# Kernel tuning notes

Hardware: AMD Instinct MI355X
Metric: run time of the kernel (lower is better)

## Reference

```python
import jax, jax.numpy as jnp
import numpy as np

B, S, D = 4, 4096, 64

def setup_inputs() -> dict:
    key = jax.random.key(0)
    kq, kk, kv, km = jax.random.split(key, 4)
    q = jax.random.normal(kq, (B, S, D), dtype=jnp.float32)
    k = jax.random.normal(kk, (B, S, D), dtype=jnp.float32)
    v = jax.random.normal(kv, (B, S, D), dtype=jnp.float32)
    # binary keep-mask in {0,1}; log(mask) -> {0, -inf}
    mask = (jax.random.uniform(km, (B, S)) > 0.2).astype(jnp.float32)
    return {"q": q, "k": k, "v": v, "mask": mask}

def reference(q, k, v, mask):
    emb_dim = q.shape[-1]
    qs = q / jnp.asarray(emb_dim, q.dtype) ** 0.5           # [B,S,D] scaled query
    scores = jnp.einsum('bqd,bkd->bqk', qs, k)              # [B,S,S]
    scores = scores + jnp.log(mask)[:, None, :]             # mask keys via log-add
    w = jax.nn.softmax(scores, axis=-1)                     # [B,S,S]
    out = jnp.einsum('bqk,bkd->bqd', w, v)                  # [B,S,D]
    # post-blend: masked query positions pass through the (scaled) query
    return out * mask[..., None] + qs * (1.0 - mask)[..., None]
```

## Files before the change

kernel.cpp:

```cpp
#include <hip/hip_runtime.h>
#include <hip/hip_bf16.h>

#define BATCH 4
#define SEQ   4096
#define DIM   64
#define TK    64
#define TOTQ  (BATCH * SEQ)
#define LOG2E 1.4426950408889634f

#if __has_builtin(__builtin_amdgcn_mfma_f32_16x16x16bf16_1k)
#define HAVE_1K 1
#else
#define HAVE_1K 0
#endif

#if __has_builtin(__builtin_amdgcn_exp2f)
#define EXP2(x) __builtin_amdgcn_exp2f(x)
#else
#define EXP2(x) exp2f(x)
#endif

typedef __attribute__((ext_vector_type(8))) short bf16x8;
typedef __attribute__((ext_vector_type(4))) short bf16x4;
typedef __attribute__((ext_vector_type(4))) float f32x4;

#define AS1 __attribute__((address_space(1)))
#define AS3 __attribute__((address_space(3)))

static __device__ __forceinline__ short f2bf(float x) {
    __hip_bfloat16 h = __float2bfloat16(x);
    return *reinterpret_cast<short*>(&h);
}
static __device__ __forceinline__ float bf2f(short s) {
    unsigned int u = ((unsigned int)(unsigned short)s) << 16;
    float f; __builtin_memcpy(&f, &u, 4); return f;
}
static __device__ __forceinline__ int pk2bf(float lo, float hi) {
    __hip_bfloat162 t = __float22bfloat162_rn(make_float2(lo, hi));
    int r; __builtin_memcpy(&r, &t, 4); return r;
}
static __device__ __forceinline__ bf16x4 mk4(const f32x4& s) {
    int2 t = make_int2(pk2bf(s[0], s[1]), pk2bf(s[2], s[3]));
    bf16x4 r; __builtin_memcpy(&r, &t, 8); return r;
}
static __device__ __forceinline__ f32x4 mfma16(bf16x4 a, bf16x4 b, f32x4 c) {
#if HAVE_1K
    return __builtin_amdgcn_mfma_f32_16x16x16bf16_1k(a, b, c, 0, 0, 0);
#else
    asm("v_mfma_f32_16x16x16_bf16 %0, %1, %2, %0" : "+v"(c) : "v"(a), "v"(b));
    return c;
#endif
}
static __device__ __forceinline__ void async16(const short* g, short* l) {
    __builtin_amdgcn_global_load_lds((const AS1 unsigned int*)g,
                                     (AS3 unsigned int*)l, 16, 0, 0);
}

__global__ __launch_bounds__(256)
void pack_kv(const float* __restrict__ kg, const float* __restrict__ vg,
             const float* __restrict__ mg,
             short* __restrict__ kp, short* __restrict__ vtp)
{
    if (blockIdx.x < 256) {
        #pragma unroll
        for (int i = 0; i < 4; ++i) {
            const int unit = blockIdx.x * 1024 + i * 256 + threadIdx.x;
            const int row = unit >> 4;
            const int d0  = (unit & 15) * 4;
            f32x4 kv = *reinterpret_cast<const f32x4*>(kg + (size_t)row * DIM + d0);
            short4 ks;
            ks.x = f2bf(kv[0]); ks.y = f2bf(kv[1]); ks.z = f2bf(kv[2]); ks.w = f2bf(kv[3]);
            const int gs = (d0 >> 3) ^ (row & 7);
            *reinterpret_cast<short4*>(kp + (size_t)row * DIM + gs * 8 + (d0 & 7)) = ks;
        }
    } else {
        __shared__ float Vl[64][66];
        __shared__ float Ml[64];
        const int tile = blockIdx.x - 256;
        const float* src = vg + (size_t)tile * TK * DIM;
        const int tid = threadIdx.x;
        #pragma unroll
        for (int i = 0; i < 4; ++i) {
            int idx = i * 256 + tid;
            int key = idx >> 4, part = idx & 15;
            f32x4 vv = *reinterpret_cast<const f32x4*>(src + (size_t)key * DIM + part * 4);
            float2* p0 = reinterpret_cast<float2*>(&Vl[key][part * 4]);
            p0[0] = make_float2(vv[0], vv[1]);
            p0[1] = make_float2(vv[2], vv[3]);
        }
        if (tid < 64) Ml[tid] = mg[(size_t)tile * TK + tid];
        __syncthreads();
        #pragma unroll
        for (int i = 0; i < 2; ++i) {
            const int gid = i * 256 + tid;
            const int d = gid >> 3;
            const int G = gid & 7;
            const int qd = G >> 1, u = G & 1;
            alignas(16) short s8[8];
            #pragma unroll
            for (int e = 0; e < 8; ++e) {
                const int v = e >> 2, j = e & 3;
                const int key = (2 * u + v) * 16 + qd * 4 + j;
                s8[e] = f2bf(Vl[key][d] * Ml[key]);
            }
            const int Gs = G ^ (d & 7);
            short* dst = vtp + (size_t)tile * (TK * DIM) + d * TK + Gs * 8;
            *reinterpret_cast<int4*>(dst) = *reinterpret_cast<const int4*>(s8);
        }
    }
}

template<int NSEG>
__global__ __launch_bounds__(256, 4)
void attn_fwd8(const float* __restrict__ qg, const float* __restrict__ mg,
               const short* __restrict__ kp, const short* __restrict__ vtp,
               float* __restrict__ outg,
               short* __restrict__ Opart, float* __restrict__ lpart)
{
    constexpr int SEGLEN = SEQ / NSEG;
    constexpr int ITERS  = SEGLEN / TK;

    __shared__ __align__(16) short Kl[2][TK][DIM];
    __shared__ __align__(16) short Vt[2][DIM][TK];

    const int tid  = threadIdx.x;
    const int wave = tid >> 6;
    const int lane = tid & 63;
    const int ln   = lane & 15;
    const int quad = lane >> 4;

    const int qblk = blockIdx.x & 31;
    const int rest = blockIdx.x >> 5;
    const int seg  = (NSEG == 1) ? 0 : (rest & (NSEG - 1));
    const int b    = (NSEG == 1) ? rest : (rest / NSEG);

    const int qw = qblk * 128 + wave * 32;
    const size_t bbase = (size_t)b * SEQ * DIM;

    const short* kb  = kp  + bbase + (size_t)seg * SEGLEN * DIM;
    const short* vb  = vtp + bbase + (size_t)seg * SEGLEN * DIM;
    const float* mgb = mg + (size_t)b * SEQ;

    const int gs0 = quad ^ (ln & 7);

    bf16x8 aq[2][2];
    #pragma unroll
    for (int qt = 0; qt < 2; ++qt) {
        const float* qrow = qg + bbase + (size_t)(qw + qt * 16 + ln) * DIM;
        #pragma unroll
        for (int h = 0; h < 2; ++h) {
            alignas(16) short tmp[8];
            #pragma unroll
            for (int j = 0; j < 8; ++j)
                tmp[j] = f2bf(qrow[quad * 8 + h * 32 + j] * (0.125f * LOG2E));
            aq[qt][h] = *reinterpret_cast<bf16x8*>(tmp);
        }
    }

    f32x4 O[2][4];
    float lacc[2] = {0.f, 0.f};
    #pragma unroll
    for (int qt = 0; qt < 2; ++qt)
        #pragma unroll
        for (int i = 0; i < 4; ++i) O[qt][i] = (f32x4){0.f, 0.f, 0.f, 0.f};

    #pragma unroll
    for (int i = 0; i < 2; ++i) {
        const int c = wave * 2 + i;
        async16(kb + c * 512 + lane * 8, &Kl[0][0][0] + c * 512);
        async16(vb + c * 512 + lane * 8, &Vt[0][0][0] + c * 512);
    }

    for (int t = 0; t < ITERS; ++t) {
        const int buf = t & 1;
        asm volatile("s_waitcnt vmcnt(0)" ::: "memory");
        __syncthreads();

        if (t + 1 < ITERS) {
            const short* gk = kb + (size_t)(t + 1) * TK * DIM;
            const short* gv = vb + (size_t)(t + 1) * TK * DIM;
            #pragma unroll
            for (int i = 0; i < 2; ++i) {
                const int c = wave * 2 + i;
                async16(gk + c * 512 + lane * 8, &Kl[buf ^ 1][0][0] + c * 512);
                async16(gv + c * 512 + lane * 8, &Vt[buf ^ 1][0][0] + c * 512);
            }
        }

        const int key0 = seg * SEGLEN + t * TK;
        const short* klb = &Kl[buf][0][0];
        const short* vtb = &Vt[buf][0][0];

        #pragma unroll
        for (int u = 0; u < 2; ++u) {
            f32x4 m4[2];
            #pragma unroll
            for (int v = 0; v < 2; ++v)
                m4[v] = *reinterpret_cast<const f32x4*>(
                    mgb + key0 + (2 * u + v) * 16 + quad * 4);

            f32x4 sf[2][2];
            #pragma unroll
            for (int v = 0; v < 2; ++v) {
                const int s = 2 * u + v;
                bf16x8 ka0 = *reinterpret_cast<const bf16x8*>(
                    klb + (s * 16 + ln) * DIM + gs0 * 8);
                bf16x8 ka1 = *reinterpret_cast<const bf16x8*>(
                    klb + (s * 16 + ln) * DIM + (gs0 ^ 4) * 8);
                #pragma unroll
                for (int qt = 0; qt < 2; ++qt) {
                    f32x4 acc = (f32x4){0.f, 0.f, 0.f, 0.f};
                    acc = __builtin_amdgcn_mfma_f32_16x16x32_bf16(ka0, aq[qt][0], acc, 0, 0, 0);
                    acc = __builtin_amdgcn_mfma_f32_16x16x32_bf16(ka1, aq[qt][1], acc, 0, 0, 0);
                    sf[qt][v] = acc;
                }
            }

            bf16x4 bp[2][2];
            #pragma unroll
            for (int qt = 0; qt < 2; ++qt) {
                #pragma unroll
                for (int v = 0; v < 2; ++v) {
                    #pragma unroll
                    for (int r = 0; r < 4; ++r) {
                        sf[qt][v][r] = EXP2(sf[qt][v][r]);
                        lacc[qt] = fmaf(sf[qt][v][r], m4[v][r], lacc[qt]);
                    }
                    bp[qt][v] = mk4(sf[qt][v]);
                }
            }

            const int gvu = (quad * 2 + u) ^ (ln & 7);
            #pragma unroll
            for (int ds = 0; ds < 4; ++ds) {
                bf16x8 vf = *reinterpret_cast<const bf16x8*>(
                    vtb + (ds * 16 + ln) * TK + gvu * 8);
                bf16x4 va0 = __builtin_shufflevector(vf, vf, 0, 1, 2, 3);
                bf16x4 va1 = __builtin_shufflevector(vf, vf, 4, 5, 6, 7);
                #pragma unroll
                for (int qt = 0; qt < 2; ++qt) {
                    O[qt][ds] = mfma16(va0, bp[qt][0], O[qt][ds]);
                    O[qt][ds] = mfma16(va1, bp[qt][1], O[qt][ds]);
                }
            }
        }
    }

    #pragma unroll
    for (int qt = 0; qt < 2; ++qt) {
        lacc[qt] += __shfl_xor(lacc[qt], 16);
        lacc[qt] += __shfl_xor(lacc[qt], 32);
    }

    if (NSEG == 1) {
        #pragma unroll
        for (int qt = 0; qt < 2; ++qt) {
            const int qrow_i = qw + qt * 16 + ln;
            const float qm = mgb[qrow_i];
            const float inv = 1.0f / lacc[qt];
            const float* qrow = qg + bbase + (size_t)qrow_i * DIM;
            float* orow = outg + bbase + (size_t)qrow_i * DIM;
            #pragma unroll
            for (int ds = 0; ds < 4; ++ds) {
                const int d0 = ds * 16 + quad * 4;
                f32x4 o4;
                #pragma unroll
                for (int r = 0; r < 4; ++r) o4[r] = O[qt][ds][r] * inv;
                if (qm == 0.0f) {
                    f32x4 q4 = *reinterpret_cast<const f32x4*>(qrow + d0);
                    #pragma unroll
                    for (int r = 0; r < 4; ++r) o4[r] = q4[r] * 0.125f;
                }
                *reinterpret_cast<f32x4*>(orow + d0) = o4;
            }
        }
    } else {
        #pragma unroll
        for (int qt = 0; qt < 2; ++qt) {
            const int gq = b * SEQ + qw + qt * 16 + ln;
            short* ob = Opart + ((size_t)seg * TOTQ + gq) * 64;
            #pragma unroll
            for (int ds = 0; ds < 2; ++ds) {
                bf16x4 lo = mk4(O[qt][ds * 2 + 0]);
                bf16x4 hi = mk4(O[qt][ds * 2 + 1]);
                *reinterpret_cast<bf16x4*>(ob + (ds * 2 + 0) * 16 + quad * 4) = lo;
                *reinterpret_cast<bf16x4*>(ob + (ds * 2 + 1) * 16 + quad * 4) = hi;
            }
            if (quad == 0) lpart[(size_t)seg * TOTQ + gq] = lacc[qt];
        }
    }
}

template<int NSEG>
__global__ __launch_bounds__(256)
void combine_p(const short* __restrict__ Opart, const float* __restrict__ lpart,
               const float* __restrict__ qg, const float* __restrict__ mg,
               float* __restrict__ outg)
{
    const int t = blockIdx.x * 256 + threadIdx.x;
    const int gq = t >> 4;
    const int d0 = (t & 15) * 4;
    float a0 = 0.f, a1 = 0.f, a2 = 0.f, a3 = 0.f, den = 0.f;
    #pragma unroll
    for (int s = 0; s < NSEG; ++s) {
        const short* ob = Opart + ((size_t)s * TOTQ + gq) * 64 + d0;
        short4 o4 = *reinterpret_cast<const short4*>(ob);
        a0 += bf2f(o4.x); a1 += bf2f(o4.y);
        a2 += bf2f(o4.z); a3 += bf2f(o4.w);
        den += lpart[(size_t)s * TOTQ + gq];
    }
    const float inv = 1.0f / den;
    f32x4 o;
    o[0] = a0 * inv; o[1] = a1 * inv; o[2] = a2 * inv; o[3] = a3 * inv;
    if (mg[gq] == 0.0f) {
        f32x4 q4 = *reinterpret_cast<const f32x4*>(qg + (size_t)gq * DIM + d0);
        #pragma unroll
        for (int r = 0; r < 4; ++r) o[r] = q4[r] * 0.125f;
    }
    *reinterpret_cast<f32x4*>(outg + (size_t)gq * DIM + d0) = o;
}

extern "C" void kernel_launch(void* const* d_in, const int* in_sizes, int n_in,
                              void* d_out, int out_size, void* d_ws, size_t ws_size,
                              hipStream_t stream) {
    (void)in_sizes; (void)n_in; (void)out_size;
    const float* q = (const float*)d_in[0];
    const float* k = (const float*)d_in[1];
    const float* v = (const float*)d_in[2];
    const float* m = (const float*)d_in[3];
    float* out = (float*)d_out;

    const size_t nelem  = (size_t)BATCH * SEQ * DIM;
    const size_t packsz = nelem * 2 * sizeof(short);
    const size_t osz    = (size_t)8 * TOTQ * 64 * sizeof(short);
    const size_t lsz    = (size_t)8 * TOTQ * sizeof(float);

    short* kp  = (short*)d_ws;
    short* vtp = kp + nelem;
    short* Op  = (short*)((char*)d_ws + packsz);
    float* lp  = (float*)((char*)d_ws + packsz + osz);

    pack_kv<<<dim3(512), dim3(256), 0, stream>>>(k, v, m, kp, vtp);

    if (ws_size >= packsz + osz + lsz) {
        attn_fwd8<8><<<dim3(BATCH * 32 * 8), dim3(256), 0, stream>>>(
            q, m, kp, vtp, out, Op, lp);
        combine_p<8><<<dim3(TOTQ * 16 / 256), dim3(256), 0, stream>>>(
            Op, lp, q, m, out);
    } else {
        attn_fwd8<1><<<dim3(BATCH * 32), dim3(256), 0, stream>>>(
            q, m, kp, vtp, out, nullptr, nullptr);
    }
}
```

Baseline: 104.9 us.

## Halve key tile to 32, double split-K segments to 16, raise occupancy

Shrinks the per-iteration key tile from 64 to 32 keys, which also changes the packed transposed-V layout and its swizzle. The number of key segments grows from 8 to 16, doubling the grid, and launch bounds now ask for 8 blocks per CU to improve occupancy and latency hiding. The trade-off is twice as many partial outputs written and read by the combine kernel, more loop iterations and barriers per key, and a larger workspace requirement.

```diff
diff --git a/kernel.cpp b/kernel.cpp
--- a/kernel.cpp
+++ b/kernel.cpp
@@ -4,8 +4,9 @@
 #define BATCH 4
 #define SEQ   4096
 #define DIM   64
-#define TK    64
+#define TK    32
 #define TOTQ  (BATCH * SEQ)
+#define NSEG  16
 #define LOG2E 1.4426950408889634f
 
 #if __has_builtin(__builtin_amdgcn_mfma_f32_16x16x16bf16_1k)
@@ -76,8 +77,8 @@
     } else {
         __shared__ float Vl[64][66];
         __shared__ float Ml[64];
-        const int tile = blockIdx.x - 256;
-        const float* src = vg + (size_t)tile * TK * DIM;
+        const int t64 = blockIdx.x - 256;
+        const float* src = vg + (size_t)t64 * 64 * DIM;
         const int tid = threadIdx.x;
         #pragma unroll
         for (int i = 0; i < 4; ++i) {
@@ -88,36 +89,36 @@
             p0[0] = make_float2(vv[0], vv[1]);
             p0[1] = make_float2(vv[2], vv[3]);
         }
-        if (tid < 64) Ml[tid] = mg[(size_t)tile * TK + tid];
+        if (tid < 64) Ml[tid] = mg[(size_t)t64 * 64 + tid];
         __syncthreads();
         #pragma unroll
         for (int i = 0; i < 2; ++i) {
             const int gid = i * 256 + tid;
-            const int d = gid >> 3;
-            const int G = gid & 7;
-            const int qd = G >> 1, u = G & 1;
+            const int t2 = gid >> 8;
+            const int d  = (gid >> 2) & 63;
+            const int G  = gid & 3;
             alignas(16) short s8[8];
             #pragma unroll
             for (int e = 0; e < 8; ++e) {
                 const int v = e >> 2, j = e & 3;
-                const int key = (2 * u + v) * 16 + qd * 4 + j;
+                const int key = t2 * 32 + v * 16 + G * 4 + j;
                 s8[e] = f2bf(Vl[key][d] * Ml[key]);
             }
-            const int Gs = G ^ (d & 7);
-            short* dst = vtp + (size_t)tile * (TK * DIM) + d * TK + Gs * 8;
+            const int Gs = G ^ ((d >> 1) & 3);
+            short* dst = vtp + ((size_t)t64 * 2 + t2) * (TK * DIM) + d * TK + Gs * 8;
             *reinterpret_cast<int4*>(dst) = *reinterpret_cast<const int4*>(s8);
         }
     }
 }
 
-template<int NSEG>
-__global__ __launch_bounds__(256, 4)
-void attn_fwd8(const float* __restrict__ qg, const float* __restrict__ mg,
+template<int NS>
+__global__ __launch_bounds__(256, 8)
+void attn_fwd9(const float* __restrict__ qg, const float* __restrict__ mg,
                const short* __restrict__ kp, const short* __restrict__ vtp,
                float* __restrict__ outg,
                short* __restrict__ Opart, float* __restrict__ lpart)
 {
-    constexpr int SEGLEN = SEQ / NSEG;
+    constexpr int SEGLEN = SEQ / NS;
     constexpr int ITERS  = SEGLEN / TK;
 
     __shared__ __align__(16) short Kl[2][TK][DIM];
@@ -131,8 +132,8 @@
 
     const int qblk = blockIdx.x & 31;
     const int rest = blockIdx.x >> 5;
-    const int seg  = (NSEG == 1) ? 0 : (rest & (NSEG - 1));
-    const int b    = (NSEG == 1) ? rest : (rest / NSEG);
+    const int seg  = (NS == 1) ? 0 : (rest & (NS - 1));
+    const int b    = (NS == 1) ? rest : (rest / NS);
 
     const int qw = qblk * 128 + wave * 32;
     const size_t bbase = (size_t)b * SEQ * DIM;
@@ -142,6 +143,7 @@
     const float* mgb = mg + (size_t)b * SEQ;
 
     const int gs0 = quad ^ (ln & 7);
+    const int gsv = quad ^ ((ln >> 1) & 3);
 
     bf16x8 aq[2][2];
     #pragma unroll
@@ -164,12 +166,8 @@
         #pragma unroll
         for (int i = 0; i < 4; ++i) O[qt][i] = (f32x4){0.f, 0.f, 0.f, 0.f};
 
-    #pragma unroll
-    for (int i = 0; i < 2; ++i) {
-        const int c = wave * 2 + i;
-        async16(kb + c * 512 + lane * 8, &Kl[0][0][0] + c * 512);
-        async16(vb + c * 512 + lane * 8, &Vt[0][0][0] + c * 512);
-    }
+    async16(kb + wave * 512 + lane * 8, &Kl[0][0][0] + wave * 512);
+    async16(vb + wave * 512 + lane * 8, &Vt[0][0][0] + wave * 512);
 
     for (int t = 0; t < ITERS; ++t) {
         const int buf = t & 1;
@@ -179,69 +177,59 @@
         if (t + 1 < ITERS) {
             const short* gk = kb + (size_t)(t + 1) * TK * DIM;
             const short* gv = vb + (size_t)(t + 1) * TK * DIM;
-            #pragma unroll
-            for (int i = 0; i < 2; ++i) {
-                const int c = wave * 2 + i;
-                async16(gk + c * 512 + lane * 8, &Kl[buf ^ 1][0][0] + c * 512);
-                async16(gv + c * 512 + lane * 8, &Vt[buf ^ 1][0][0] + c * 512);
-            }
+            async16(gk + wave * 512 + lane * 8, &Kl[buf ^ 1][0][0] + wave * 512);
+            async16(gv + wave * 512 + lane * 8, &Vt[buf ^ 1][0][0] + wave * 512);
         }
 
         const int key0 = seg * SEGLEN + t * TK;
         const short* klb = &Kl[buf][0][0];
         const short* vtb = &Vt[buf][0][0];
 
-        #pragma unroll
-        for (int u = 0; u < 2; ++u) {
-            f32x4 m4[2];
-            #pragma unroll
-            for (int v = 0; v < 2; ++v)
-                m4[v] = *reinterpret_cast<const f32x4*>(
-                    mgb + key0 + (2 * u + v) * 16 + quad * 4);
-
-            f32x4 sf[2][2];
+        f32x4 m4[2];
+        #pragma unroll
+        for (int v = 0; v < 2; ++v)
+            m4[v] = *reinterpret_cast<const f32x4*>(mgb + key0 + v * 16 + quad * 4);
+
+        f32x4 sf[2][2];
+        #pragma unroll
+        for (int v = 0; v < 2; ++v) {
+            bf16x8 ka0 = *reinterpret_cast<const bf16x8*>(
+                klb + (v * 16 + ln) * DIM + gs0 * 8);
+            bf16x8 ka1 = *reinterpret_cast<const bf16x8*>(
+                klb + (v * 16 + ln) * DIM + (gs0 ^ 4) * 8);
+            #pragma unroll
+            for (int qt = 0; qt < 2; ++qt) {
+                f32x4 acc = (f32x4){0.f, 0.f, 0.f, 0.f};
+                acc = __builtin_amdgcn_mfma_f32_16x16x32_bf16(ka0, aq[qt][0], acc, 0, 0, 0);
+                acc = __builtin_amdgcn_mfma_f32_16x16x32_bf16(ka1, aq[qt][1], acc, 0, 0, 0);
+                sf[qt][v] = acc;
+            }
+        }
+
+        bf16x4 bp[2][2];
+        #pragma unroll
+        for (int qt = 0; qt < 2; ++qt) {
             #pragma unroll
             for (int v = 0; v < 2; ++v) {
-                const int s = 2 * u + v;
-                bf16x8 ka0 = *reinterpret_cast<const bf16x8*>(
-                    klb + (s * 16 + ln) * DIM + gs0 * 8);
-                bf16x8 ka1 = *reinterpret_cast<const bf16x8*>(
-                    klb + (s * 16 + ln) * DIM + (gs0 ^ 4) * 8);
                 #pragma unroll
-                for (int qt = 0; qt < 2; ++qt) {
-                    f32x4 acc = (f32x4){0.f, 0.f, 0.f, 0.f};
-                    acc = __builtin_amdgcn_mfma_f32_16x16x32_bf16(ka0, aq[qt][0], acc, 0, 0, 0);
-                    acc = __builtin_amdgcn_mfma_f32_16x16x32_bf16(ka1, aq[qt][1], acc, 0, 0, 0);
-                    sf[qt][v] = acc;
+                for (int r = 0; r < 4; ++r) {
+                    sf[qt][v][r] = EXP2(sf[qt][v][r]);
+                    lacc[qt] = fmaf(sf[qt][v][r], m4[v][r], lacc[qt]);
                 }
-            }
-
-            bf16x4 bp[2][2];
+                bp[qt][v] = mk4(sf[qt][v]);
+            }
+        }
+
+        #pragma unroll
+        for (int ds = 0; ds < 4; ++ds) {
+            bf16x8 vf = *reinterpret_cast<const bf16x8*>(
+                vtb + (ds * 16 + ln) * TK + gsv * 8);
+            bf16x4 va0 = __builtin_shufflevector(vf, vf, 0, 1, 2, 3);
+            bf16x4 va1 = __builtin_shufflevector(vf, vf, 4, 5, 6, 7);
             #pragma unroll
             for (int qt = 0; qt < 2; ++qt) {
-                #pragma unroll
-                for (int v = 0; v < 2; ++v) {
-                    #pragma unroll
-                    for (int r = 0; r < 4; ++r) {
-                        sf[qt][v][r] = EXP2(sf[qt][v][r]);
-                        lacc[qt] = fmaf(sf[qt][v][r], m4[v][r], lacc[qt]);
-                    }
-                    bp[qt][v] = mk4(sf[qt][v]);
-                }
-            }
-
-            const int gvu = (quad * 2 + u) ^ (ln & 7);
-            #pragma unroll
-            for (int ds = 0; ds < 4; ++ds) {
-                bf16x8 vf = *reinterpret_cast<const bf16x8*>(
-                    vtb + (ds * 16 + ln) * TK + gvu * 8);
-                bf16x4 va0 = __builtin_shufflevector(vf, vf, 0, 1, 2, 3);
-                bf16x4 va1 = __builtin_shufflevector(vf, vf, 4, 5, 6, 7);
-                #pragma unroll
-                for (int qt = 0; qt < 2; ++qt) {
-                    O[qt][ds] = mfma16(va0, bp[qt][0], O[qt][ds]);
-                    O[qt][ds] = mfma16(va1, bp[qt][1], O[qt][ds]);
-                }
+                O[qt][ds] = mfma16(va0, bp[qt][0], O[qt][ds]);
+                O[qt][ds] = mfma16(va1, bp[qt][1], O[qt][ds]);
             }
         }
     }
@@ -252,7 +240,7 @@
         lacc[qt] += __shfl_xor(lacc[qt], 32);
     }
 
-    if (NSEG == 1) {
+    if (NS == 1) {
         #pragma unroll
         for (int qt = 0; qt < 2; ++qt) {
             const int qrow_i = qw + qt * 16 + ln;
@@ -291,7 +279,7 @@
     }
 }
 
-template<int NSEG>
+template<int NS>
 __global__ __launch_bounds__(256)
 void combine_p(const short* __restrict__ Opart, const float* __restrict__ lpart,
                const float* __restrict__ qg, const float* __restrict__ mg,
@@ -302,7 +290,7 @@
     const int d0 = (t & 15) * 4;
     float a0 = 0.f, a1 = 0.f, a2 = 0.f, a3 = 0.f, den = 0.f;
     #pragma unroll
-    for (int s = 0; s < NSEG; ++s) {
+    for (int s = 0; s < NS; ++s) {
         const short* ob = Opart + ((size_t)s * TOTQ + gq) * 64 + d0;
         short4 o4 = *reinterpret_cast<const short4*>(ob);
         a0 += bf2f(o4.x); a1 += bf2f(o4.y);
@@ -332,8 +320,8 @@
 
     const size_t nelem  = (size_t)BATCH * SEQ * DIM;
     const size_t packsz = nelem * 2 * sizeof(short);
-    const size_t osz    = (size_t)8 * TOTQ * 64 * sizeof(short);
-    const size_t lsz    = (size_t)8 * TOTQ * sizeof(float);
+    const size_t osz    = (size_t)NSEG * TOTQ * 64 * sizeof(short);
+    const size_t lsz    = (size_t)NSEG * TOTQ * sizeof(float);
 
     short* kp  = (short*)d_ws;
     short* vtp = kp + nelem;
@@ -343,12 +331,12 @@
     pack_kv<<<dim3(512), dim3(256), 0, stream>>>(k, v, m, kp, vtp);
 
     if (ws_size >= packsz + osz + lsz) {
-        attn_fwd8<8><<<dim3(BATCH * 32 * 8), dim3(256), 0, stream>>>(
+        attn_fwd9<NSEG><<<dim3(BATCH * 32 * NSEG), dim3(256), 0, stream>>>(
             q, m, kp, vtp, out, Op, lp);
-        combine_p<8><<<dim3(TOTQ * 16 / 256), dim3(256), 0, stream>>>(
+        combine_p<NSEG><<<dim3(TOTQ * 16 / 256), dim3(256), 0, stream>>>(
             Op, lp, q, m, out);
     } else {
-        attn_fwd8<1><<<dim3(BATCH * 32), dim3(256), 0, stream>>>(
+        attn_fwd9<1><<<dim3(BATCH * 32), dim3(256), 0, stream>>>(
             q, m, kp, vtp, out, nullptr, nullptr);
     }
 }
```

Result: slower. 230.2 us (+119.4%).

## Split keys into 16 segments, stage whole segment in LDS at once

Applied to the files above, without the earlier changes.

Raises the key split from 8 to 16 segments, so each block handles 256 keys. It loads that block's whole K/V segment (64 KB) into LDS with one wait and barrier, replacing the double-buffered per-tile loop. Block indices are remapped so blocks that share a segment are adjacent, which may improve L2 reuse, and the partial-output store is repacked into 16-byte writes with a matching combine layout. The cost is twice the partial-output traffic in combine, occupancy capped at two blocks per CU by the LDS footprint, and no overlap of loads with compute inside a block.

```diff
diff --git a/kernel.cpp b/kernel.cpp
--- a/kernel.cpp
+++ b/kernel.cpp
@@ -5,6 +5,9 @@
 #define SEQ   4096
 #define DIM   64
 #define TK    64
+#define NSEG  16
+#define SEGLEN (SEQ / NSEG)
+#define ITERS  (SEGLEN / TK)
 #define TOTQ  (BATCH * SEQ)
 #define LOG2E 1.4426950408889634f
 
@@ -77,7 +80,7 @@
         __shared__ float Vl[64][66];
         __shared__ float Ml[64];
         const int tile = blockIdx.x - 256;
-        const float* src = vg + (size_t)tile * TK * DIM;
+        const float* src = vg + (size_t)tile * 64 * DIM;
         const int tid = threadIdx.x;
         #pragma unroll
         for (int i = 0; i < 4; ++i) {
@@ -88,7 +91,7 @@
             p0[0] = make_float2(vv[0], vv[1]);
             p0[1] = make_float2(vv[2], vv[3]);
         }
-        if (tid < 64) Ml[tid] = mg[(size_t)tile * TK + tid];
+        if (tid < 64) Ml[tid] = mg[(size_t)tile * 64 + tid];
         __syncthreads();
         #pragma unroll
         for (int i = 0; i < 2; ++i) {
@@ -104,24 +107,19 @@
                 s8[e] = f2bf(Vl[key][d] * Ml[key]);
             }
             const int Gs = G ^ (d & 7);
-            short* dst = vtp + (size_t)tile * (TK * DIM) + d * TK + Gs * 8;
+            short* dst = vtp + (size_t)tile * (64 * DIM) + d * 64 + Gs * 8;
             *reinterpret_cast<int4*>(dst) = *reinterpret_cast<const int4*>(s8);
         }
     }
 }
 
-template<int NSEG>
-__global__ __launch_bounds__(256, 4)
-void attn_fwd8(const float* __restrict__ qg, const float* __restrict__ mg,
-               const short* __restrict__ kp, const short* __restrict__ vtp,
-               float* __restrict__ outg,
-               short* __restrict__ Opart, float* __restrict__ lpart)
+__global__ __launch_bounds__(256, 2)
+void attn_seg(const float* __restrict__ qg, const float* __restrict__ mg,
+              const short* __restrict__ kp, const short* __restrict__ vtp,
+              short* __restrict__ Opart, float* __restrict__ lpart)
 {
-    constexpr int SEGLEN = SEQ / NSEG;
-    constexpr int ITERS  = SEGLEN / TK;
-
-    __shared__ __align__(16) short Kl[2][TK][DIM];
-    __shared__ __align__(16) short Vt[2][DIM][TK];
+    __shared__ __align__(16) short Ks[SEGLEN * DIM];
+    __shared__ __align__(16) short Vs[ITERS * DIM * TK];
 
     const int tid  = threadIdx.x;
     const int wave = tid >> 6;
@@ -129,10 +127,10 @@
     const int ln   = lane & 15;
     const int quad = lane >> 4;
 
-    const int qblk = blockIdx.x & 31;
-    const int rest = blockIdx.x >> 5;
-    const int seg  = (NSEG == 1) ? 0 : (rest & (NSEG - 1));
-    const int b    = (NSEG == 1) ? rest : (rest / NSEG);
+    const int x = blockIdx.x;
+    const int seg  = (x & 7) | ((x >> 10) << 3);
+    const int qblk = (x >> 3) & 31;
+    const int b    = (x >> 8) & 3;
 
     const int qw = qblk * 128 + wave * 32;
     const size_t bbase = (size_t)b * SEQ * DIM;
@@ -165,31 +163,18 @@
         for (int i = 0; i < 4; ++i) O[qt][i] = (f32x4){0.f, 0.f, 0.f, 0.f};
 
     #pragma unroll
-    for (int i = 0; i < 2; ++i) {
-        const int c = wave * 2 + i;
-        async16(kb + c * 512 + lane * 8, &Kl[0][0][0] + c * 512);
-        async16(vb + c * 512 + lane * 8, &Vt[0][0][0] + c * 512);
-    }
+    for (int i = 0; i < 8; ++i) {
+        const int c = wave * 8 + i;
+        async16(kb + c * 512 + lane * 8, Ks + c * 512);
+        async16(vb + c * 512 + lane * 8, Vs + c * 512);
+    }
+    asm volatile("s_waitcnt vmcnt(0)" ::: "memory");
+    __syncthreads();
 
     for (int t = 0; t < ITERS; ++t) {
-        const int buf = t & 1;
-        asm volatile("s_waitcnt vmcnt(0)" ::: "memory");
-        __syncthreads();
-
-        if (t + 1 < ITERS) {
-            const short* gk = kb + (size_t)(t + 1) * TK * DIM;
-            const short* gv = vb + (size_t)(t + 1) * TK * DIM;
-            #pragma unroll
-            for (int i = 0; i < 2; ++i) {
-                const int c = wave * 2 + i;
-                async16(gk + c * 512 + lane * 8, &Kl[buf ^ 1][0][0] + c * 512);
-                async16(gv + c * 512 + lane * 8, &Vt[buf ^ 1][0][0] + c * 512);
-            }
-        }
-
+        const short* klb = Ks + t * (TK * DIM);
+        const short* vtb = Vs + t * (TK * DIM);
         const int key0 = seg * SEGLEN + t * TK;
-        const short* klb = &Kl[buf][0][0];
-        const short* vtb = &Vt[buf][0][0];
 
         #pragma unroll
         for (int u = 0; u < 2; ++u) {
@@ -250,60 +235,36 @@
     for (int qt = 0; qt < 2; ++qt) {
         lacc[qt] += __shfl_xor(lacc[qt], 16);
         lacc[qt] += __shfl_xor(lacc[qt], 32);
-    }
-
-    if (NSEG == 1) {
-        #pragma unroll
-        for (int qt = 0; qt < 2; ++qt) {
-            const int qrow_i = qw + qt * 16 + ln;
-            const float qm = mgb[qrow_i];
-            const float inv = 1.0f / lacc[qt];
-            const float* qrow = qg + bbase + (size_t)qrow_i * DIM;
-            float* orow = outg + bbase + (size_t)qrow_i * DIM;
-            #pragma unroll
-            for (int ds = 0; ds < 4; ++ds) {
-                const int d0 = ds * 16 + quad * 4;
-                f32x4 o4;
-                #pragma unroll
-                for (int r = 0; r < 4; ++r) o4[r] = O[qt][ds][r] * inv;
-                if (qm == 0.0f) {
-                    f32x4 q4 = *reinterpret_cast<const f32x4*>(qrow + d0);
-                    #pragma unroll
-                    for (int r = 0; r < 4; ++r) o4[r] = q4[r] * 0.125f;
-                }
-                *reinterpret_cast<f32x4*>(orow + d0) = o4;
-            }
-        }
-    } else {
-        #pragma unroll
-        for (int qt = 0; qt < 2; ++qt) {
-            const int gq = b * SEQ + qw + qt * 16 + ln;
-            short* ob = Opart + ((size_t)seg * TOTQ + gq) * 64;
-            #pragma unroll
-            for (int ds = 0; ds < 2; ++ds) {
-                bf16x4 lo = mk4(O[qt][ds * 2 + 0]);
-                bf16x4 hi = mk4(O[qt][ds * 2 + 1]);
-                *reinterpret_cast<bf16x4*>(ob + (ds * 2 + 0) * 16 + quad * 4) = lo;
-                *reinterpret_cast<bf16x4*>(ob + (ds * 2 + 1) * 16 + quad * 4) = hi;
-            }
-            if (quad == 0) lpart[(size_t)seg * TOTQ + gq] = lacc[qt];
-        }
-    }
-}
-
-template<int NSEG>
+        const int gq = b * SEQ + qw + qt * 16 + ln;
+        short* ob = Opart + ((size_t)seg * TOTQ + gq) * 64 + quad * 16;
+        bf16x4 f0 = mk4(O[qt][0]), f1 = mk4(O[qt][1]);
+        bf16x4 f2 = mk4(O[qt][2]), f3 = mk4(O[qt][3]);
+        alignas(16) short w0[8], w1[8];
+        *reinterpret_cast<bf16x4*>(w0)     = f0;
+        *reinterpret_cast<bf16x4*>(w0 + 4) = f1;
+        *reinterpret_cast<bf16x4*>(w1)     = f2;
+        *reinterpret_cast<bf16x4*>(w1 + 4) = f3;
+        *reinterpret_cast<int4*>(ob)     = *reinterpret_cast<const int4*>(w0);
+        *reinterpret_cast<int4*>(ob + 8) = *reinterpret_cast<const int4*>(w1);
+        if (quad == 0) lpart[(size_t)seg * TOTQ + gq] = lacc[qt];
+    }
+}
+
 __global__ __launch_bounds__(256)
-void combine_p(const short* __restrict__ Opart, const float* __restrict__ lpart,
-               const float* __restrict__ qg, const float* __restrict__ mg,
-               float* __restrict__ outg)
+void combine_p16(const short* __restrict__ Opart, const float* __restrict__ lpart,
+                 const float* __restrict__ qg, const float* __restrict__ mg,
+                 float* __restrict__ outg)
 {
     const int t = blockIdx.x * 256 + threadIdx.x;
     const int gq = t >> 4;
     const int d0 = (t & 15) * 4;
+    const int ds = d0 >> 4;
+    const int qd = (d0 >> 2) & 3;
+    const int off = qd * 16 + ds * 4;
     float a0 = 0.f, a1 = 0.f, a2 = 0.f, a3 = 0.f, den = 0.f;
     #pragma unroll
     for (int s = 0; s < NSEG; ++s) {
-        const short* ob = Opart + ((size_t)s * TOTQ + gq) * 64 + d0;
+        const short* ob = Opart + ((size_t)s * TOTQ + gq) * 64 + off;
         short4 o4 = *reinterpret_cast<const short4*>(ob);
         a0 += bf2f(o4.x); a1 += bf2f(o4.y);
         a2 += bf2f(o4.z); a3 += bf2f(o4.w);
@@ -318,6 +279,140 @@
         for (int r = 0; r < 4; ++r) o[r] = q4[r] * 0.125f;
     }
     *reinterpret_cast<f32x4*>(outg + (size_t)gq * DIM + d0) = o;
+}
+
+__global__ __launch_bounds__(256, 4)
+void attn_fb(const float* __restrict__ qg, const float* __restrict__ mg,
+             const short* __restrict__ kp, const short* __restrict__ vtp,
+             float* __restrict__ outg)
+{
+    __shared__ __align__(16) short Kl[2][TK][DIM];
+    __shared__ __align__(16) short Vt[2][DIM][TK];
+    const int tid  = threadIdx.x;
+    const int wave = tid >> 6;
+    const int lane = tid & 63;
+    const int ln   = lane & 15;
+    const int quad = lane >> 4;
+    const int qblk = blockIdx.x & 31;
+    const int b    = blockIdx.x >> 5;
+    const int qw = qblk * 128 + wave * 32;
+    const size_t bbase = (size_t)b * SEQ * DIM;
+    const short* kb  = kp  + bbase;
+    const short* vb  = vtp + bbase;
+    const float* mgb = mg + (size_t)b * SEQ;
+    const int gs0 = quad ^ (ln & 7);
+
+    bf16x8 aq[2][2];
+    #pragma unroll
+    for (int qt = 0; qt < 2; ++qt) {
+        const float* qrow = qg + bbase + (size_t)(qw + qt * 16 + ln) * DIM;
+        #pragma unroll
+        for (int h = 0; h < 2; ++h) {
+            alignas(16) short tmp[8];
+            #pragma unroll
+            for (int j = 0; j < 8; ++j)
+                tmp[j] = f2bf(qrow[quad * 8 + h * 32 + j] * (0.125f * LOG2E));
+            aq[qt][h] = *reinterpret_cast<bf16x8*>(tmp);
+        }
+    }
+    f32x4 O[2][4];
+    float lacc[2] = {0.f, 0.f};
+    #pragma unroll
+    for (int qt = 0; qt < 2; ++qt)
+        #pragma unroll
+        for (int i = 0; i < 4; ++i) O[qt][i] = (f32x4){0.f, 0.f, 0.f, 0.f};
+    #pragma unroll
+    for (int i = 0; i < 2; ++i) {
+        const int c = wave * 2 + i;
+        async16(kb + c * 512 + lane * 8, &Kl[0][0][0] + c * 512);
+        async16(vb + c * 512 + lane * 8, &Vt[0][0][0] + c * 512);
+    }
+    for (int t = 0; t < SEQ / TK; ++t) {
+        const int buf = t & 1;
+        asm volatile("s_waitcnt vmcnt(0)" ::: "memory");
+        __syncthreads();
+        if (t + 1 < SEQ / TK) {
+            const short* gk = kb + (size_t)(t + 1) * TK * DIM;
+            const short* gv = vb + (size_t)(t + 1) * TK * DIM;
+            #pragma unroll
+            for (int i = 0; i < 2; ++i) {
+                const int c = wave * 2 + i;
+                async16(gk + c * 512 + lane * 8, &Kl[buf ^ 1][0][0] + c * 512);
+                async16(gv + c * 512 + lane * 8, &Vt[buf ^ 1][0][0] + c * 512);
+            }
+        }
+        const int key0 = t * TK;
+        const short* klb = &Kl[buf][0][0];
+        const short* vtb = &Vt[buf][0][0];
+        #pragma unroll
+        for (int u = 0; u < 2; ++u) {
+            f32x4 m4[2];
+            #pragma unroll
+            for (int v = 0; v < 2; ++v)
+                m4[v] = *reinterpret_cast<const f32x4*>(mgb + key0 + (2 * u + v) * 16 + quad * 4);
+            f32x4 sf[2][2];
+            #pragma unroll
+            for (int v = 0; v < 2; ++v) {
+                const int s = 2 * u + v;
+                bf16x8 ka0 = *reinterpret_cast<const bf16x8*>(klb + (s * 16 + ln) * DIM + gs0 * 8);
+                bf16x8 ka1 = *reinterpret_cast<const bf16x8*>(klb + (s * 16 + ln) * DIM + (gs0 ^ 4) * 8);
+                #pragma unroll
+                for (int qt = 0; qt < 2; ++qt) {
+                    f32x4 acc = (f32x4){0.f, 0.f, 0.f, 0.f};
+                    acc = __builtin_amdgcn_mfma_f32_16x16x32_bf16(ka0, aq[qt][0], acc, 0, 0, 0);
+                    acc = __builtin_amdgcn_mfma_f32_16x16x32_bf16(ka1, aq[qt][1], acc, 0, 0, 0);
+                    sf[qt][v] = acc;
+                }
+            }
+            bf16x4 bp[2][2];
+            #pragma unroll
+            for (int qt = 0; qt < 2; ++qt)
+                #pragma unroll
+                for (int v = 0; v < 2; ++v) {
+                    #pragma unroll
+                    for (int r = 0; r < 4; ++r) {
+                        sf[qt][v][r] = EXP2(sf[qt][v][r]);
+                        lacc[qt] = fmaf(sf[qt][v][r], m4[v][r], lacc[qt]);
+                    }
+                    bp[qt][v] = mk4(sf[qt][v]);
+                }
+            const int gvu = (quad * 2 + u) ^ (ln & 7);
+            #pragma unroll
+            for (int ds = 0; ds < 4; ++ds) {
+                bf16x8 vf = *reinterpret_cast<const bf16x8*>(vtb + (ds * 16 + ln) * TK + gvu * 8);
+                bf16x4 va0 = __builtin_shufflevector(vf, vf, 0, 1, 2, 3);
+                bf16x4 va1 = __builtin_shufflevector(vf, vf, 4, 5, 6, 7);
+                #pragma unroll
+                for (int qt = 0; qt < 2; ++qt) {
+                    O[qt][ds] = mfma16(va0, bp[qt][0], O[qt][ds]);
+                    O[qt][ds] = mfma16(va1, bp[qt][1], O[qt][ds]);
+                }
+            }
+        }
+    }
+    #pragma unroll
+    for (int qt = 0; qt < 2; ++qt) {
+        lacc[qt] += __shfl_xor(lacc[qt], 16);
+        lacc[qt] += __shfl_xor(lacc[qt], 32);
+        const int qrow_i = qw + qt * 16 + ln;
+        const float qm = mgb[qrow_i];
+        const float inv = 1.0f / lacc[qt];
+        const float* qrow = qg + bbase + (size_t)qrow_i * DIM;
+        float* orow = outg + bbase + (size_t)qrow_i * DIM;
+        #pragma unroll
+        for (int ds = 0; ds < 4; ++ds) {
+            const int d0 = ds * 16 + quad * 4;
+            f32x4 o4;
+            #pragma unroll
+            for (int r = 0; r < 4; ++r) o4[r] = O[qt][ds][r] * inv;
+            if (qm == 0.0f) {
+                f32x4 q4 = *reinterpret_cast<const f32x4*>(qrow + d0);
+                #pragma unroll
+                for (int r = 0; r < 4; ++r) o4[r] = q4[r] * 0.125f;
+            }
+            *reinterpret_cast<f32x4*>(orow + d0) = o4;
+        }
+    }
 }
 
 extern "C" void kernel_launch(void* const* d_in, const int* in_sizes, int n_in,
@@ -332,8 +427,8 @@
 
     const size_t nelem  = (size_t)BATCH * SEQ * DIM;
     const size_t packsz = nelem * 2 * sizeof(short);
-    const size_t osz    = (size_t)8 * TOTQ * 64 * sizeof(short);
-    const size_t lsz    = (size_t)8 * TOTQ * sizeof(float);
+    const size_t osz    = (size_t)NSEG * TOTQ * 64 * sizeof(short);
+    const size_t lsz    = (size_t)NSEG * TOTQ * sizeof(float);
 
     short* kp  = (short*)d_ws;
     short* vtp = kp + nelem;
@@ -343,12 +438,12 @@
     pack_kv<<<dim3(512), dim3(256), 0, stream>>>(k, v, m, kp, vtp);
 
     if (ws_size >= packsz + osz + lsz) {
-        attn_fwd8<8><<<dim3(BATCH * 32 * 8), dim3(256), 0, stream>>>(
-            q, m, kp, vtp, out, Op, lp);
-        combine_p<8><<<dim3(TOTQ * 16 / 256), dim3(256), 0, stream>>>(
+        attn_seg<<<dim3(BATCH * 32 * NSEG), dim3(256), 0, stream>>>(
+            q, m, kp, vtp, Op, lp);
+        combine_p16<<<dim3(TOTQ * 16 / 256), dim3(256), 0, stream>>>(
             Op, lp, q, m, out);
     } else {
-        attn_fwd8<1><<<dim3(BATCH * 32), dim3(256), 0, stream>>>(
-            q, m, kp, vtp, out, nullptr, nullptr);
-    }
-}
+        attn_fb<<<dim3(BATCH * 32), dim3(256), 0, stream>>>(
+            q, m, kp, vtp, out);
+    }
+}
```

New measurement: 109.8 us. 1.05x slower.
